# Performance work log

Measured on AMD Instinct MI355X. Metric: run time of the kernel, lower is better.

## Reference

```python
import jax, jax.numpy as jnp
import numpy as np
from jax import lax

WIN = 9
PAD = WIN // 2
WIN_SIZE = float(WIN ** 3)
EPS = 1e-5


def _box_sum3d(x):
    """Sliding-window sum with an all-ones 9x9x9 kernel, zero padding, stride 1.
    Implemented as three separable 1D convolutions (exactly equal to the dense
    conv3d with a ones kernel). x: [N, C, D, H, W]."""
    dn = ('NCDHW', 'OIDHW', 'NCDHW')
    kD = jnp.ones((1, 1, WIN, 1, 1), x.dtype)
    kH = jnp.ones((1, 1, 1, WIN, 1), x.dtype)
    kW = jnp.ones((1, 1, 1, 1, WIN), x.dtype)
    x = lax.conv_general_dilated(x, kD, (1, 1, 1), [(PAD, PAD), (0, 0), (0, 0)], dimension_numbers=dn)
    x = lax.conv_general_dilated(x, kH, (1, 1, 1), [(0, 0), (PAD, PAD), (0, 0)], dimension_numbers=dn)
    x = lax.conv_general_dilated(x, kW, (1, 1, 1), [(0, 0), (0, 0), (PAD, PAD)], dimension_numbers=dn)
    return x


def setup_inputs() -> dict:
    key = jax.random.key(0)
    k1, k2 = jax.random.split(key)
    shape = (1, 1, 192, 192, 192)
    y_true = jax.random.uniform(k1, shape, dtype=jnp.float32)
    y_pred = jax.random.uniform(k2, shape, dtype=jnp.float32)
    return {"y_true": y_true, "y_pred": y_pred}


def reference(y_true, y_pred):
    Ii, Ji = y_true, y_pred
    I_sum = _box_sum3d(Ii)
    J_sum = _box_sum3d(Ji)
    I2_sum = _box_sum3d(Ii * Ii)
    J2_sum = _box_sum3d(Ji * Ji)
    IJ_sum = _box_sum3d(Ii * Ji)

    u_I = I_sum / WIN_SIZE
    u_J = J_sum / WIN_SIZE

    cross = IJ_sum - u_J * I_sum - u_I * J_sum + u_I * u_J * WIN_SIZE
    I_var = I2_sum - 2.0 * u_I * I_sum + u_I * u_I * WIN_SIZE
    J_var = J2_sum - 2.0 * u_J * J_sum + u_J * u_J * WIN_SIZE

    cc = cross * cross / (I_var * J_var + EPS)
    return -jnp.mean(cc)
```

## Files before the change

### kernel.cpp

```cpp
#include <hip/hip_runtime.h>
#include <hip/hip_fp16.h>

#define DIMN 192
#define SD (DIMN * DIMN)
#define CS (DIMN * DIMN * DIMN)
#define WIN_F 729.0f
#define NPART 768

typedef unsigned int uint32;

__device__ __forceinline__ float2 up32(uint32 u) {
    __half2 h = *(__half2*)&u;
    return __half22float2(h);
}
__device__ __forceinline__ uint32 pk32(float x, float y) {
    __half2 h = __floats2half2_rn(x, y);
    return *(uint32*)&h;
}

__global__ __launch_bounds__(256) void k1_d(const float* __restrict__ I,
                                            const float* __restrict__ J,
                                            uint2* __restrict__ s0123,
                                            __half* __restrict__ s4) {
    const int chunk = blockIdx.x / 144;
    const int hw = (blockIdx.x % 144) * 256 + threadIdx.x;
    const int d0 = chunk * 24;

    float ri[9], rj[9];
#pragma unroll
    for (int k = 0; k < 9; k++) { ri[k] = 0.f; rj[k] = 0.f; }
    float r0 = 0.f, r1 = 0.f, r2 = 0.f, r3 = 0.f, r4 = 0.f;

    for (int i = 0; i < 32; i++) {
        const int ds = d0 - 4 + i;
        float iv = 0.f, jv = 0.f;
        if ((unsigned)ds < DIMN) {
            iv = I[ds * SD + hw];
            jv = J[ds * SD + hw];
        }
        const float oi = ri[0], oj = rj[0];
        r0 += iv - oi;
        r1 += jv - oj;
        r2 += iv * iv - oi * oi;
        r3 += jv * jv - oj * oj;
        r4 += iv * jv - oi * oj;
#pragma unroll
        for (int k = 0; k < 8; k++) { ri[k] = ri[k + 1]; rj[k] = rj[k + 1]; }
        ri[8] = iv;
        rj[8] = jv;

        if (i >= 8) {
            const int o = (d0 + i - 8) * SD + hw;
            s0123[o] = make_uint2(pk32(r0, r1), pk32(r2, r3));
            s4[o] = __float2half_rn(r4);
        }
    }
}

__global__ __launch_bounds__(256) void k2_hwcc(const uint2* __restrict__ s0123,
                                               const __half* __restrict__ s4,
                                               double* __restrict__ partials) {
    const int tid = threadIdx.x;
    const int l = tid & 63;
    const int wg = blockIdx.x * 4 + (tid >> 6);
    const int wseg = wg & 1;
    const int band = (wg >> 1) & 7;
    const int d = wg >> 4;
    const int h0 = band * 24;
    const int w0 = -4 + wseg * 72;
    const int we = w0 + 2 * l;
    const bool pok = ((unsigned)we < DIMN);
    const int lo = wseg * 96;
    const bool f = pok && (we >= lo) && (we < lo + 96);
    const int cb = d * SD + we;

    float re0 = 0.f, re1 = 0.f, re2 = 0.f, re3 = 0.f, re4 = 0.f;
    float ro0 = 0.f, ro1 = 0.f, ro2 = 0.f, ro3 = 0.f, ro4 = 0.f;
    double acc = 0.0;

    for (int i = 0; i < 32; ++i) {
        const int hh = h0 - 4 + i;
        uint4 qa = make_uint4(0u, 0u, 0u, 0u);
        uint32 qa4 = 0u;
        if (pok && (unsigned)hh < DIMN) {
            const int o = cb + hh * DIMN;
            qa = *(const uint4*)(s0123 + o);
            qa4 = *(const uint32*)(s4 + o);
        }
        uint4 qs = make_uint4(0u, 0u, 0u, 0u);
        uint32 qs4 = 0u;
        const int hd = hh - 9;
        if (i >= 9 && pok && (unsigned)hd < DIMN) {
            const int o = cb + hd * DIMN;
            qs = *(const uint4*)(s0123 + o);
            qs4 = *(const uint32*)(s4 + o);
        }
        float2 t;
        t = up32(qa.x); re0 += t.x; re1 += t.y;
        t = up32(qs.x); re0 -= t.x; re1 -= t.y;
        t = up32(qa.y); re2 += t.x; re3 += t.y;
        t = up32(qs.y); re2 -= t.x; re3 -= t.y;
        t = up32(qa.z); ro0 += t.x; ro1 += t.y;
        t = up32(qs.z); ro0 -= t.x; ro1 -= t.y;
        t = up32(qa.w); ro2 += t.x; ro3 += t.y;
        t = up32(qs.w); ro2 -= t.x; ro3 -= t.y;
        t = up32(qa4);  re4 += t.x; ro4 += t.y;
        t = up32(qs4);  re4 -= t.x; ro4 -= t.y;

        if (i >= 8) {
            float Se[5], So[5];
#define WTAP(c, rE, rO)                                                       \
            {                                                                 \
                const uint32 tc = pk32(rE, rO);                               \
                const float2 m2 = up32((uint32)__shfl((int)tc, l - 2, 64));   \
                const float2 m1 = up32((uint32)__shfl((int)tc, l - 1, 64));   \
                const float2 p1 = up32((uint32)__shfl((int)tc, l + 1, 64));   \
                const float2 p2 = up32((uint32)__shfl((int)tc, l + 2, 64));   \
                const float M = m1.x + m1.y + rE + rO + p1.x + p1.y;          \
                Se[c] = M + m2.x + m2.y + p2.x;                               \
                So[c] = M + m2.y + p2.x + p2.y;                               \
            }
            WTAP(0, re0, ro0)
            WTAP(1, re1, ro1)
            WTAP(2, re2, ro2)
            WTAP(3, re3, ro3)
            WTAP(4, re4, ro4)
#undef WTAP
            if (f) {
                {
                    const float u_I = Se[0] / WIN_F;
                    const float u_J = Se[1] / WIN_F;
                    const float cross = Se[4] - u_J * Se[0] - u_I * Se[1] + u_I * u_J * WIN_F;
                    const float I_var = Se[2] - 2.0f * u_I * Se[0] + u_I * u_I * WIN_F;
                    const float J_var = Se[3] - 2.0f * u_J * Se[1] + u_J * u_J * WIN_F;
                    acc += (double)(cross * cross / (I_var * J_var + 1e-5f));
                }
                {
                    const float u_I = So[0] / WIN_F;
                    const float u_J = So[1] / WIN_F;
                    const float cross = So[4] - u_J * So[0] - u_I * So[1] + u_I * u_J * WIN_F;
                    const float I_var = So[2] - 2.0f * u_I * So[0] + u_I * u_I * WIN_F;
                    const float J_var = So[3] - 2.0f * u_J * So[1] + u_J * u_J * WIN_F;
                    acc += (double)(cross * cross / (I_var * J_var + 1e-5f));
                }
            }
        }
    }

    __shared__ double wred[4];
#pragma unroll
    for (int off = 32; off > 0; off >>= 1) acc += __shfl_down(acc, off, 64);
    if ((tid & 63) == 0) wred[tid >> 6] = acc;
    __syncthreads();
    if (tid == 0) partials[blockIdx.x] = wred[0] + wred[1] + wred[2] + wred[3];
}

__global__ void k_final(const double* __restrict__ partials, float* __restrict__ out) {
    __shared__ double wred[4];
    double acc = 0.0;
    for (int i = threadIdx.x; i < NPART; i += 256) acc += partials[i];
#pragma unroll
    for (int off = 32; off > 0; off >>= 1) acc += __shfl_down(acc, off, 64);
    if ((threadIdx.x & 63) == 0) wred[threadIdx.x >> 6] = acc;
    __syncthreads();
    if (threadIdx.x == 0) {
        const double total = wred[0] + wred[1] + wred[2] + wred[3];
        out[0] = -(float)(total / (double)CS);
    }
}

extern "C" void kernel_launch(void* const* d_in, const int* in_sizes, int n_in,
                              void* d_out, int out_size, void* d_ws, size_t ws_size,
                              hipStream_t stream) {
    const float* I = (const float*)d_in[0];
    const float* J = (const float*)d_in[1];
    char* ws = (char*)d_ws;
    uint2*  s0123 = (uint2*)ws;
    __half* s4    = (__half*)(ws + (size_t)CS * 8);
    double* partials = (double*)(ws + (size_t)CS * 10);
    float* out = (float*)d_out;

    hipLaunchKernelGGL(k1_d, dim3(1152), dim3(256), 0, stream, I, J, s0123, s4);
    hipLaunchKernelGGL(k2_hwcc, dim3(768), dim3(256), 0, stream,
                       (const uint2*)s0123, (const __half*)s4, partials);
    hipLaunchKernelGGL(k_final, dim3(1), dim3(256), 0, stream, partials, out);
}
```

Baseline: 157.0 us.

## Halve k2 H-bands for more blocks and fuse final reduction via atomics

Splits each k2 wave's H range into 12-row bands instead of 24, doubling the grid to 1536 blocks for more parallelism. The cost is more redundant halo loads (20 rows loaded per 12 outputs). The separate final-reduction kernel is removed: blocks atomically add into a double accumulator, and the last block (tracked by a counter) writes the output. A memset is added to zero the accumulator and counter, and the atomic double add makes the summation order nondeterministic.

```diff
diff --git a/kernel.cpp b/kernel.cpp
--- a/kernel.cpp
+++ b/kernel.cpp
@@ -5,7 +5,7 @@
 #define SD (DIMN * DIMN)
 #define CS (DIMN * DIMN * DIMN)
 #define WIN_F 729.0f
-#define NPART 768
+#define NBLK2 1536
 
 typedef unsigned int uint32;
 
@@ -59,16 +59,17 @@
 
 __global__ __launch_bounds__(256) void k2_hwcc(const uint2* __restrict__ s0123,
                                                const __half* __restrict__ s4,
-                                               double* __restrict__ partials) {
+                                               double* __restrict__ accum,
+                                               uint32* __restrict__ counter,
+                                               float* __restrict__ out) {
     const int tid = threadIdx.x;
     const int l = tid & 63;
     const int wg = blockIdx.x * 4 + (tid >> 6);
     const int wseg = wg & 1;
-    const int band = (wg >> 1) & 7;
-    const int d = wg >> 4;
-    const int h0 = band * 24;
-    const int w0 = -4 + wseg * 72;
-    const int we = w0 + 2 * l;
+    const int band = (wg >> 1) & 15;
+    const int d = wg >> 5;
+    const int h0 = band * 12;
+    const int we = -4 + wseg * 72 + 2 * l;
     const bool pok = ((unsigned)we < DIMN);
     const int lo = wseg * 96;
     const bool f = pok && (we >= lo) && (we < lo + 96);
@@ -78,7 +79,7 @@
     float ro0 = 0.f, ro1 = 0.f, ro2 = 0.f, ro3 = 0.f, ro4 = 0.f;
     double acc = 0.0;
 
-    for (int i = 0; i < 32; ++i) {
+    for (int i = 0; i < 20; ++i) {
         const int hh = h0 - 4 + i;
         uint4 qa = make_uint4(0u, 0u, 0u, 0u);
         uint32 qa4 = 0u;
@@ -152,20 +153,16 @@
     for (int off = 32; off > 0; off >>= 1) acc += __shfl_down(acc, off, 64);
     if ((tid & 63) == 0) wred[tid >> 6] = acc;
     __syncthreads();
-    if (tid == 0) partials[blockIdx.x] = wred[0] + wred[1] + wred[2] + wred[3];
-}
-
-__global__ void k_final(const double* __restrict__ partials, float* __restrict__ out) {
-    __shared__ double wred[4];
-    double acc = 0.0;
-    for (int i = threadIdx.x; i < NPART; i += 256) acc += partials[i];
-#pragma unroll
-    for (int off = 32; off > 0; off >>= 1) acc += __shfl_down(acc, off, 64);
-    if ((threadIdx.x & 63) == 0) wred[threadIdx.x >> 6] = acc;
-    __syncthreads();
-    if (threadIdx.x == 0) {
-        const double total = wred[0] + wred[1] + wred[2] + wred[3];
-        out[0] = -(float)(total / (double)CS);
+    if (tid == 0) {
+        const double bsum = wred[0] + wred[1] + wred[2] + wred[3];
+        atomicAdd(accum, bsum);
+        __threadfence();
+        const uint32 old = atomicAdd(counter, 1u);
+        if (old == NBLK2 - 1) {
+            __threadfence();
+            const double total = atomicAdd(accum, 0.0);
+            out[0] = -(float)(total / (double)CS);
+        }
     }
 }
 
@@ -177,11 +174,12 @@
     char* ws = (char*)d_ws;
     uint2*  s0123 = (uint2*)ws;
     __half* s4    = (__half*)(ws + (size_t)CS * 8);
-    double* partials = (double*)(ws + (size_t)CS * 10);
+    double* accum = (double*)(ws + (size_t)CS * 10);
+    uint32* counter = (uint32*)(ws + (size_t)CS * 10 + 8);
     float* out = (float*)d_out;
 
+    hipMemsetAsync(ws + (size_t)CS * 10, 0, 16, stream);
     hipLaunchKernelGGL(k1_d, dim3(1152), dim3(256), 0, stream, I, J, s0123, s4);
-    hipLaunchKernelGGL(k2_hwcc, dim3(768), dim3(256), 0, stream,
-                       (const uint2*)s0123, (const __half*)s4, partials);
-    hipLaunchKernelGGL(k_final, dim3(1), dim3(256), 0, stream, partials, out);
+    hipLaunchKernelGGL(k2_hwcc, dim3(NBLK2), dim3(256), 0, stream,
+                       (const uint2*)s0123, (const __half*)s4, accum, counter, out);
 }
```

Result: slower. 186.2 us (+18.6%).
